# Kernel optimization log

Hardware: AMD Instinct MI355X
Metric: run time of the kernel (lower is better)

The kernel has to match this reference:

```python
import jax, jax.numpy as jnp
import numpy as np

N = 20000        # genes
E = 100000       # edges per relation
D_IN = 512
HID = 64         # hidden_dim (per-head channels in layers 0,1)
HEADS = 8
D_H = HID * HEADS   # 512 hidden width
D_OUT = 256
NEG_SLOPE = 0.2  # GATv2Conv default negative_slope


def _gatv2(x, src, dst, Wl, bl, Wr, br, att, out_bias, heads, ch):
    """PyG GATv2Conv, add_self_loops=False, concat=True, eval mode (no dropout)."""
    n = x.shape[0]
    xl = (x @ Wl + bl).reshape(n, heads, ch)   # lin_l (source transform)
    xr = (x @ Wr + br).reshape(n, heads, ch)   # lin_r (target transform)
    e = jax.nn.leaky_relu(xl[src] + xr[dst], NEG_SLOPE)   # [E,H,C]
    score = jnp.einsum('ehc,hc->eh', e, att)              # [E,H]
    # segment softmax over incoming edges of each destination node
    m = jax.ops.segment_max(score, dst, num_segments=n)   # [N,H]
    w = jnp.exp(score - m[dst])
    z = jax.ops.segment_sum(w, dst, num_segments=n)
    alpha = w / z[dst]
    out = jax.ops.segment_sum(alpha[:, :, None] * xl[src], dst, num_segments=n)
    return out.reshape(n, heads * ch) + out_bias


def _layernorm(x, g, b):
    mu = x.mean(-1, keepdims=True)
    var = x.var(-1, keepdims=True)
    return (x - mu) * jax.lax.rsqrt(var + 1e-5) * g + b


def setup_inputs() -> dict:
    key = jax.random.key(0)
    ks = jax.random.split(key, 12)
    gn = lambda k, shape, fan_in: (jax.random.normal(k, shape, dtype=jnp.float32)
                                   / np.float32(np.sqrt(fan_in)))
    inp = {}
    inp['x'] = jax.random.normal(ks[0], (N, D_IN), dtype=jnp.float32)
    inp['edge_index'] = jax.random.randint(ks[1], (3, 2, E), 0, N, dtype=jnp.int32)
    # input projection  Linear(512 -> 512)
    inp['proj_w'] = gn(ks[2], (D_IN, D_H), D_IN)
    inp['proj_b'] = jnp.zeros((D_H,), jnp.float32)
    # layers 0,1: stacked over [layer, edge_type]
    inp['l01_lin_l_w'] = gn(ks[3], (2, 3, D_H, D_H), D_H)
    inp['l01_lin_l_b'] = jnp.zeros((2, 3, D_H), jnp.float32)
    inp['l01_lin_r_w'] = gn(ks[4], (2, 3, D_H, D_H), D_H)
    inp['l01_lin_r_b'] = jnp.zeros((2, 3, D_H), jnp.float32)
    inp['l01_att'] = gn(ks[5], (2, 3, HEADS, HID), HID)
    inp['l01_bias'] = jnp.zeros((2, 3, D_H), jnp.float32)
    # layer 2: heads=1, out_channels=256, stacked over edge_type
    inp['l2_lin_l_w'] = gn(ks[6], (3, D_H, D_OUT), D_H)
    inp['l2_lin_l_b'] = jnp.zeros((3, D_OUT), jnp.float32)
    inp['l2_lin_r_w'] = gn(ks[7], (3, D_H, D_OUT), D_H)
    inp['l2_lin_r_b'] = jnp.zeros((3, D_OUT), jnp.float32)
    inp['l2_att'] = gn(ks[8], (3, 1, D_OUT), D_OUT)
    inp['l2_bias'] = jnp.zeros((3, D_OUT), jnp.float32)
    # LayerNorms
    inp['ln01_gamma'] = jnp.ones((2, D_H), jnp.float32)
    inp['ln01_beta'] = jnp.zeros((2, D_H), jnp.float32)
    inp['ln2_gamma'] = jnp.ones((D_OUT,), jnp.float32)
    inp['ln2_beta'] = jnp.zeros((D_OUT,), jnp.float32)
    return inp


def reference(x, edge_index, proj_w, proj_b,
              l01_lin_l_w, l01_lin_l_b, l01_lin_r_w, l01_lin_r_b, l01_att, l01_bias,
              l2_lin_l_w, l2_lin_l_b, l2_lin_r_w, l2_lin_r_b, l2_att, l2_bias,
              ln01_gamma, ln01_beta, ln2_gamma, ln2_beta):
    # input proj + ELU (dropout = identity in eval)
    h = jax.nn.elu(x @ proj_w + proj_b)
    # layers 0 and 1: HeteroConv(sum over 3 relations), ELU, residual, LayerNorm
    for li in range(2):
        res = h
        out = 0.0
        for et in range(3):
            src, dst = edge_index[et, 0], edge_index[et, 1]
            out = out + _gatv2(h, src, dst,
                               l01_lin_l_w[li, et], l01_lin_l_b[li, et],
                               l01_lin_r_w[li, et], l01_lin_r_b[li, et],
                               l01_att[li, et], l01_bias[li, et], HEADS, HID)
        h = jax.nn.elu(out) + res
        h = _layernorm(h, ln01_gamma[li], ln01_beta[li])
    # layer 2: heads=1, out=256; no residual (dims differ)
    out = 0.0
    for et in range(3):
        src, dst = edge_index[et, 0], edge_index[et, 1]
        out = out + _gatv2(h, src, dst,
                           l2_lin_l_w[et], l2_lin_l_b[et],
                           l2_lin_r_w[et], l2_lin_r_b[et],
                           l2_att[et], l2_bias[et], 1, D_OUT)
    h = jax.nn.elu(out)
    return _layernorm(h, ln2_gamma, ln2_beta)
```

## Files before the change

### kernel.cpp

```cpp
#include <hip/hip_runtime.h>


#define NN 20000
#define NE 100000
#define DH 512
#define DOUT 256

typedef __attribute__((ext_vector_type(8))) short short8;
typedef __attribute__((ext_vector_type(4))) short short4v;
typedef __attribute__((ext_vector_type(4))) float f32x4;

__device__ __forceinline__ float b2f(unsigned short s) {
    union { unsigned u; float f; } v; v.u = ((unsigned)s) << 16; return v.f;
}
__device__ __forceinline__ unsigned short f2b(float f) {
    unsigned u = __float_as_uint(f);
    u += 0x7FFFu + ((u >> 16) & 1u);
    return (unsigned short)(u >> 16);
}
__device__ __forceinline__ void load_lds16(const unsigned short* g, unsigned short* l) {
    __builtin_amdgcn_global_load_lds(
        (const __attribute__((address_space(1))) unsigned int*)g,
        (__attribute__((address_space(3))) unsigned int*)l, 16, 0, 0);
}

__global__ void cvt_f2b_k(const float* __restrict__ in,
                          unsigned short* __restrict__ out, int n) {
    int i0 = (blockIdx.x * blockDim.x + threadIdx.x) * 8;
    if (i0 >= n) return;
    #pragma unroll
    for (int j = 0; j < 8; j++) out[i0 + j] = f2b(in[i0 + j]);
}

__global__ void transpose_f2b_k(const float* __restrict__ in,
                                unsigned short* __restrict__ out, int R, int C,
                                long inStride, long outStride) {
    __shared__ float tile[32][33];
    in  += (size_t)blockIdx.z * inStride;
    out += (size_t)blockIdx.z * outStride;
    int c0 = blockIdx.x * 32, r0 = blockIdx.y * 32;
    int tx = threadIdx.x & 31, ty = threadIdx.x >> 5;
    #pragma unroll
    for (int i = ty; i < 32; i += 8)
        tile[i][tx] = in[(size_t)(r0 + i) * C + c0 + tx];
    __syncthreads();
    #pragma unroll
    for (int i = ty; i < 32; i += 8)
        out[(size_t)(c0 + i) * R + r0 + tx] = f2b(tile[tx][i]);
}

__global__ void count_k(const int* __restrict__ dst, int* __restrict__ counts, int E) {
    int i = blockIdx.x * blockDim.x + threadIdx.x;
    if (i < E) atomicAdd(&counts[dst[i]], 1);
}

__global__ __launch_bounds__(1024)
void scan_par_k(const int* __restrict__ counts, int* __restrict__ offs, int n) {
    __shared__ int part[1024];
    const int* c = counts + (size_t)blockIdx.x * (n + 1);
    int* o = offs + (size_t)blockIdx.x * (n + 1);
    int tid = threadIdx.x;
    int per = (n + 1023) / 1024;
    int base = tid * per;
    int lim = min(base + per, n);
    int sum = 0;
    for (int i = base; i < lim; i++) sum += c[i];
    part[tid] = sum;
    __syncthreads();
    #pragma unroll
    for (int off = 1; off < 1024; off <<= 1) {
        int v = (tid >= off) ? part[tid - off] : 0;
        __syncthreads();
        part[tid] += v;
        __syncthreads();
    }
    int run = part[tid] - sum;
    for (int i = base; i < lim; i++) { o[i] = run; run += c[i]; }
    if (tid == 1023) o[n] = part[1023];
}

__global__ void scatter_k(const int* __restrict__ src, const int* __restrict__ dst,
                          int* __restrict__ cursor, int* __restrict__ srcs_sorted, int E) {
    int i = blockIdx.x * blockDim.x + threadIdx.x;
    if (i < E) {
        int p = atomicAdd(&cursor[dst[i]], 1);
        srcs_sorted[p] = src[i];
    }
}

template<int ACT, int SEGL2>
__global__ __launch_bounds__(256)
void gemm_k(const unsigned short* __restrict__ A,
            const unsigned short* __restrict__ Bt,
            const float* __restrict__ lb,
            const float* __restrict__ rb,
            unsigned short* __restrict__ Cb,
            int M, int N, int K, int MT, int NT, int STRIPE) {
    __shared__ unsigned short As[128 * 64];
    __shared__ unsigned short Bs[128 * 64];
    int bid = blockIdx.x;
    int xcd = bid & 7, r = bid >> 3;
    int mtile = xcd * STRIPE + r / NT;
    int ntile = r % NT;
    if (mtile >= MT) return;
    int bm0 = mtile * 128, bn0 = ntile * 128;

    int tid = threadIdx.x;
    int lane = tid & 63, wave = tid >> 6;
    int quad = lane >> 4, l16 = lane & 15;
    int rw = (wave >> 1) * 64, cw = (wave & 1) * 64;
    int rxor = l16 & 7;

    f32x4 acc[4][4];
    #pragma unroll
    for (int mi = 0; mi < 4; mi++)
        #pragma unroll
        for (int ni = 0; ni < 4; ni++) acc[mi][ni] = (f32x4){0.f, 0.f, 0.f, 0.f};

    for (int k0 = 0; k0 < K; k0 += 64) {
        #pragma unroll
        for (int i = 0; i < 4; i++) {
            int f = i * 256 + tid;
            int row = f >> 3, s = f & 7;
            int cg = s ^ (row & 7);
            load_lds16(A + (size_t)(bm0 + row) * K + k0 + cg * 8, As + f * 8);
        }
        #pragma unroll
        for (int i = 0; i < 4; i++) {
            int f = i * 256 + tid;
            int col = f >> 3, s = f & 7;
            int cg = s ^ (col & 7);
            load_lds16(Bt + (size_t)(bn0 + col) * K + k0 + cg * 8, Bs + f * 8);
        }
        __syncthreads();
        #pragma unroll
        for (int ki = 0; ki < 64; ki += 32) {
            int kch = quad + (ki >> 3);
            int slot = kch ^ rxor;
            short8 af[4], bf[4];
            #pragma unroll
            for (int mi = 0; mi < 4; mi++)
                af[mi] = *(const short8*)(As + (rw + mi * 16 + l16) * 64 + slot * 8);
            #pragma unroll
            for (int ni = 0; ni < 4; ni++)
                bf[ni] = *(const short8*)(Bs + (cw + ni * 16 + l16) * 64 + slot * 8);
            #pragma unroll
            for (int mi = 0; mi < 4; mi++)
                #pragma unroll
                for (int ni = 0; ni < 4; ni++)
                    acc[mi][ni] = __builtin_amdgcn_mfma_f32_16x16x32_bf16(
                        af[mi], bf[ni], acc[mi][ni], 0, 0, 0);
        }
        __syncthreads();
    }
    #pragma unroll
    for (int mi = 0; mi < 4; mi++) {
        int orow0 = bm0 + rw + mi * 16 + quad * 4;
        #pragma unroll
        for (int ni = 0; ni < 4; ni++) {
            int col = bn0 + cw + ni * 16 + l16;
            int seg = col >> (SEGL2 + 1);
            int lr = (col >> SEGL2) & 1;
            int cc = col & ((1 << SEGL2) - 1);
            float bv = (lr ? rb : lb)[(seg << SEGL2) + cc];
            #pragma unroll
            for (int i = 0; i < 4; i++) {
                int row = orow0 + i;
                if (row >= M) continue;
                float v = acc[mi][ni][i] + bv;
                if (ACT == 1) v = v > 0.f ? v : expm1f(v);
                Cb[(size_t)row * N + col] = f2b(v);
            }
        }
    }
}

__global__ __launch_bounds__(256)
void gat_fused01_k(const unsigned short* __restrict__ C,
                   const int* __restrict__ offs3,
                   const int* __restrict__ srcs3,
                   const float* __restrict__ att,
                   const float* __restrict__ bias3,
                   unsigned short* __restrict__ hb,
                   const float* __restrict__ gamma,
                   const float* __restrict__ beta,
                   int n_nodes) {
    const unsigned LD = 3072;
    __shared__ float red[4][2];
    int tid = threadIdx.x;
    int lane = tid & 63, wave = tid >> 6;
    int half = wave & 1;
    int n = blockIdx.x * 2 + (wave >> 1);
    int c0 = half * 256 + lane * 4;
    float tot[4] = {0.f, 0.f, 0.f, 0.f};

    #pragma unroll
    for (int et = 0; et < 3; et++) {
        const int* offs = offs3 + et * (NN + 1);
        const int* srcs = srcs3 + (size_t)et * NE;
        int e0 = offs[n], e1 = offs[n + 1];
        if (e0 == e1) continue;
        const unsigned short* XL = C + et * 1024 + c0;
        float xr[4], at[4];
        {
            short4v t = *(const short4v*)(C + (size_t)n * LD + et * 1024 + 512 + c0);
            #pragma unroll
            for (int j = 0; j < 4; j++) xr[j] = b2f((unsigned short)t[j]);
            #pragma unroll
            for (int j = 0; j < 4; j++) at[j] = att[et * 512 + c0 + j];
        }
        float z = 0.f, acc[4] = {0.f, 0.f, 0.f, 0.f};
        short4v p0 = *(const short4v*)(XL + (unsigned)srcs[e0] * LD);
        short4v p1 = (e0 + 1 < e1) ? *(const short4v*)(XL + (unsigned)srcs[e0 + 1] * LD) : p0;
        for (int e = e0; e < e1; e++) {
            short4v cur = p0;
            p0 = p1;
            if (e + 2 < e1) p1 = *(const short4v*)(XL + (unsigned)srcs[e + 2] * LD);
            float xl[4];
            #pragma unroll
            for (int j = 0; j < 4; j++) xl[j] = b2f((unsigned short)cur[j]);
            float p = 0.f;
            #pragma unroll
            for (int j = 0; j < 4; j++) {
                float v = xl[j] + xr[j];
                v = v > 0.f ? v : 0.2f * v;
                p += v * at[j];
            }
            p += __shfl_xor(p, 1, 64);
            p += __shfl_xor(p, 2, 64);
            p += __shfl_xor(p, 4, 64);
            p += __shfl_xor(p, 8, 64);
            float wgt = __expf(p);
            z += wgt;
            #pragma unroll
            for (int j = 0; j < 4; j++) acc[j] += wgt * xl[j];
        }
        float inv = 1.f / z;
        #pragma unroll
        for (int j = 0; j < 4; j++) tot[j] += acc[j] * inv;
    }

    unsigned short* hrow = hb + (size_t)n * DH + c0;
    float v[4]; float s1 = 0.f;
    {
        short4v rt = *(const short4v*)hrow;
        #pragma unroll
        for (int j = 0; j < 4; j++) {
            int c = c0 + j;
            float x = tot[j] + bias3[c] + bias3[512 + c] + bias3[1024 + c];
            x = x > 0.f ? x : expm1f(x);
            x += b2f((unsigned short)rt[j]);
            v[j] = x; s1 += x;
        }
    }
    #pragma unroll
    for (int off = 1; off < 64; off <<= 1) s1 += __shfl_xor(s1, off, 64);
    if (lane == 0) red[wave][0] = s1;
    __syncthreads();
    float s1full = s1 + red[wave ^ 1][0];
    float mean = s1full * (1.f / DH);
    float s2 = 0.f;
    #pragma unroll
    for (int j = 0; j < 4; j++) { float d = v[j] - mean; s2 += d * d; }
    #pragma unroll
    for (int off = 1; off < 64; off <<= 1) s2 += __shfl_xor(s2, off, 64);
    if (lane == 0) red[wave][1] = s2;
    __syncthreads();
    float s2full = s2 + red[wave ^ 1][1];
    float rstd = rsqrtf(s2full * (1.f / DH) + 1e-5f);
    unsigned short ov[4];
    #pragma unroll
    for (int j = 0; j < 4; j++) {
        int c = c0 + j;
        ov[j] = f2b((v[j] - mean) * rstd * gamma[c] + beta[c]);
    }
    *(short4v*)hrow = (short4v){(short)ov[0], (short)ov[1], (short)ov[2], (short)ov[3]};
}

__global__ void gat_fused2_k(const unsigned short* __restrict__ C,
                             const int* __restrict__ offs3,
                             const int* __restrict__ srcs3,
                             const float* __restrict__ att,
                             const float* __restrict__ bias3,
                             const float* __restrict__ gamma,
                             const float* __restrict__ beta,
                             float* __restrict__ out, int n_nodes) {
    const unsigned LD = 1536;
    int lane = threadIdx.x & 63;
    int n = blockIdx.x * (blockDim.x >> 6) + (threadIdx.x >> 6);
    if (n >= n_nodes) return;
    int c0 = lane * 4;
    float tot[4] = {0.f, 0.f, 0.f, 0.f};

    #pragma unroll
    for (int et = 0; et < 3; et++) {
        const int* offs = offs3 + et * (NN + 1);
        const int* srcs = srcs3 + (size_t)et * NE;
        int e0 = offs[n], e1 = offs[n + 1];
        if (e0 == e1) continue;
        const unsigned short* XL = C + et * 512 + c0;
        float xr[4], at[4];
        {
            short4v t = *(const short4v*)(C + (size_t)n * LD + et * 512 + 256 + c0);
            #pragma unroll
            for (int j = 0; j < 4; j++) xr[j] = b2f((unsigned short)t[j]);
            #pragma unroll
            for (int j = 0; j < 4; j++) at[j] = att[et * 256 + c0 + j];
        }
        float z = 0.f, acc[4] = {0.f, 0.f, 0.f, 0.f};
        short4v p0 = *(const short4v*)(XL + (unsigned)srcs[e0] * LD);
        short4v p1 = (e0 + 1 < e1) ? *(const short4v*)(XL + (unsigned)srcs[e0 + 1] * LD) : p0;
        for (int e = e0; e < e1; e++) {
            short4v cur = p0;
            p0 = p1;
            if (e + 2 < e1) p1 = *(const short4v*)(XL + (unsigned)srcs[e + 2] * LD);
            float xl[4];
            #pragma unroll
            for (int j = 0; j < 4; j++) xl[j] = b2f((unsigned short)cur[j]);
            float p = 0.f;
            #pragma unroll
            for (int j = 0; j < 4; j++) {
                float v = xl[j] + xr[j];
                v = v > 0.f ? v : 0.2f * v;
                p += v * at[j];
            }
            #pragma unroll
            for (int off = 1; off < 64; off <<= 1) p += __shfl_xor(p, off, 64);
            float wgt = __expf(p);
            z += wgt;
            #pragma unroll
            for (int j = 0; j < 4; j++) acc[j] += wgt * xl[j];
        }
        float inv = 1.f / z;
        #pragma unroll
        for (int j = 0; j < 4; j++) tot[j] += acc[j] * inv;
    }

    float v[4]; float s1 = 0.f;
    #pragma unroll
    for (int j = 0; j < 4; j++) {
        int c = c0 + j;
        float x = tot[j] + bias3[c] + bias3[256 + c] + bias3[512 + c];
        x = x > 0.f ? x : expm1f(x);
        v[j] = x; s1 += x;
    }
    #pragma unroll
    for (int off = 1; off < 64; off <<= 1) s1 += __shfl_xor(s1, off, 64);
    float mean = s1 * (1.f / DOUT);
    float s2 = 0.f;
    #pragma unroll
    for (int j = 0; j < 4; j++) { float d = v[j] - mean; s2 += d * d; }
    #pragma unroll
    for (int off = 1; off < 64; off <<= 1) s2 += __shfl_xor(s2, off, 64);
    float rstd = rsqrtf(s2 * (1.f / DOUT) + 1e-5f);
    #pragma unroll
    for (int j = 0; j < 4; j++) {
        int c = c0 + j;
        out[(size_t)n * DOUT + c] = (v[j] - mean) * rstd * gamma[c] + beta[c];
    }
}

extern "C" void kernel_launch(void* const* d_in, const int* in_sizes, int n_in,
                              void* d_out, int out_size, void* d_ws, size_t ws_size,
                              hipStream_t stream) {
    const float* x       = (const float*)d_in[0];
    const int*   ei      = (const int*)d_in[1];
    const float* proj_w  = (const float*)d_in[2];
    const float* proj_b  = (const float*)d_in[3];
    const float* l01lw   = (const float*)d_in[4];
    const float* l01lb   = (const float*)d_in[5];
    const float* l01rw   = (const float*)d_in[6];
    const float* l01rb   = (const float*)d_in[7];
    const float* l01att  = (const float*)d_in[8];
    const float* l01bias = (const float*)d_in[9];
    const float* l2lw    = (const float*)d_in[10];
    const float* l2lb    = (const float*)d_in[11];
    const float* l2rw    = (const float*)d_in[12];
    const float* l2rb    = (const float*)d_in[13];
    const float* l2att   = (const float*)d_in[14];
    const float* l2bias  = (const float*)d_in[15];
    const float* g01     = (const float*)d_in[16];
    const float* b01     = (const float*)d_in[17];
    const float* g2      = (const float*)d_in[18];
    const float* b2      = (const float*)d_in[19];
    (void)in_sizes; (void)n_in; (void)out_size; (void)ws_size;

    char* w = (char*)d_ws;
    size_t off = 0;
    auto carve = [&](size_t bytes) { void* p = w + off; off = (off + bytes + 255) & ~(size_t)255; return p; };
    unsigned short* h_b     = (unsigned short*)carve((size_t)NN * DH * 2);
    unsigned short* xb      = (unsigned short*)carve((size_t)NN * DH * 2);
    unsigned short* Cbuf    = (unsigned short*)carve((size_t)NN * 3072 * 2);
    unsigned short* Wt      = (unsigned short*)carve((size_t)4194304 * 2);
    int*            counts3 = (int*)           carve((size_t)3 * (NN + 1) * 4);
    int*            offs3   = (int*)           carve((size_t)3 * (NN + 1) * 4);
    int*            srcs3   = (int*)           carve((size_t)3 * NE * 4);
    carve(65536);

    unsigned short* Wt_proj = Wt;
    unsigned short* Wt_L0   = Wt_proj + 262144;
    unsigned short* Wt_L1   = Wt_L0 + 3072 * 512;
    unsigned short* Wt_L2   = Wt_L1 + 3072 * 512;

    dim3 tb(256);
    const int MT = (NN + 127) / 128;
    const int STRIPE = (MT + 7) / 8;

    cvt_f2b_k<<<dim3(5000), tb, 0, stream>>>(x, xb, NN * DH);
    transpose_f2b_k<<<dim3(16, 16, 1), tb, 0, stream>>>(proj_w, Wt_proj, 512, 512, 0, 0);
    for (int li = 0; li < 2; li++) {
        unsigned short* base = li ? Wt_L1 : Wt_L0;
        transpose_f2b_k<<<dim3(16, 16, 3), tb, 0, stream>>>(
            l01lw + (size_t)li * 3 * 262144, base, 512, 512, 262144, 2 * 262144);
        transpose_f2b_k<<<dim3(16, 16, 3), tb, 0, stream>>>(
            l01rw + (size_t)li * 3 * 262144, base + 262144, 512, 512, 262144, 2 * 262144);
    }
    transpose_f2b_k<<<dim3(8, 16, 3), tb, 0, stream>>>(
        l2lw, Wt_L2, 512, 256, 131072, 2 * 131072);
    transpose_f2b_k<<<dim3(8, 16, 3), tb, 0, stream>>>(
        l2rw, Wt_L2 + 131072, 512, 256, 131072, 2 * 131072);

    hipMemsetAsync(counts3, 0, (size_t)3 * (NN + 1) * 4, stream);
    for (int et = 0; et < 3; et++) {
        const int* dst = ei + (size_t)et * 2 * NE + NE;
        count_k<<<dim3((NE + 255) / 256), tb, 0, stream>>>(dst, counts3 + et * (NN + 1), NE);
    }
    scan_par_k<<<dim3(3), dim3(1024), 0, stream>>>(counts3, offs3, NN);
    hipMemcpyAsync(counts3, offs3, (size_t)3 * (NN + 1) * 4,
                   hipMemcpyDeviceToDevice, stream);
    for (int et = 0; et < 3; et++) {
        const int* src = ei + (size_t)et * 2 * NE;
        const int* dst = src + NE;
        scatter_k<<<dim3((NE + 255) / 256), tb, 0, stream>>>(
            src, dst, counts3 + et * (NN + 1), srcs3 + (size_t)et * NE, NE);
    }

    gemm_k<1, 9><<<dim3(8 * STRIPE * 4), tb, 0, stream>>>(
        xb, Wt_proj, proj_b, proj_b, h_b, NN, 512, 512, MT, 4, STRIPE);

    for (int li = 0; li < 2; li++) {
        gemm_k<0, 9><<<dim3(8 * STRIPE * 24), tb, 0, stream>>>(
            h_b, li ? Wt_L1 : Wt_L0,
            l01lb + (size_t)li * 3 * 512, l01rb + (size_t)li * 3 * 512,
            Cbuf, NN, 3072, 512, MT, 24, STRIPE);
        gat_fused01_k<<<dim3(NN / 2), tb, 0, stream>>>(
            Cbuf, offs3, srcs3,
            l01att + (size_t)li * 3 * 512, l01bias + (size_t)li * 3 * 512,
            h_b, g01 + (size_t)li * DH, b01 + (size_t)li * DH, NN);
    }

    gemm_k<0, 8><<<dim3(8 * STRIPE * 12), tb, 0, stream>>>(
        h_b, Wt_L2, l2lb, l2rb, Cbuf, NN, 1536, 512, MT, 12, STRIPE);
    gat_fused2_k<<<dim3(NN / 4), tb, 0, stream>>>(
        Cbuf, offs3, srcs3, l2att, l2bias, g2, b2, (float*)d_out, NN);
}
```

Before: 766.5 us.

## Batch weight transposes and CSR builds into single launches; stage GEMM stores via LDS

Merges the many per-weight transpose launches into one table-driven kernel, and folds the per-relation count and scatter launches into single kernels covering all three relations. This is meant to cut kernel launch overhead in the preprocessing phase. The GEMM epilogue now writes bf16 results into a padded LDS tile and stores rows back with 16-byte vector writes instead of scattered 2-byte stores. That should improve write coalescing, at the cost of a larger shared buffer (about 34 KB) and an extra barrier.

```diff
diff --git a/kernel.cpp b/kernel.cpp
--- a/kernel.cpp
+++ b/kernel.cpp
@@ -32,26 +32,33 @@
     for (int j = 0; j < 8; j++) out[i0 + j] = f2b(in[i0 + j]);
 }
 
-__global__ void transpose_f2b_k(const float* __restrict__ in,
-                                unsigned short* __restrict__ out, int R, int C,
-                                long inStride, long outStride) {
+struct TSeg { const float* in; unsigned short* out; int C; };
+struct TTable { TSeg s[19]; };
+
+__global__ void transpose_all_k(TTable t) {
     __shared__ float tile[32][33];
-    in  += (size_t)blockIdx.z * inStride;
-    out += (size_t)blockIdx.z * outStride;
-    int c0 = blockIdx.x * 32, r0 = blockIdx.y * 32;
+    TSeg d = t.s[blockIdx.y];
+    int tiles_x = d.C >> 5;
+    int nt = tiles_x << 4;
+    if ((int)blockIdx.x >= nt) return;
+    int bx = blockIdx.x % tiles_x, by = blockIdx.x / tiles_x;
+    int c0 = bx * 32, r0 = by * 32;
     int tx = threadIdx.x & 31, ty = threadIdx.x >> 5;
     #pragma unroll
     for (int i = ty; i < 32; i += 8)
-        tile[i][tx] = in[(size_t)(r0 + i) * C + c0 + tx];
+        tile[i][tx] = d.in[(size_t)(r0 + i) * d.C + c0 + tx];
     __syncthreads();
     #pragma unroll
     for (int i = ty; i < 32; i += 8)
-        out[(size_t)(c0 + i) * R + r0 + tx] = f2b(tile[tx][i]);
-}
-
-__global__ void count_k(const int* __restrict__ dst, int* __restrict__ counts, int E) {
+        d.out[(size_t)(c0 + i) * 512 + r0 + tx] = f2b(tile[tx][i]);
+}
+
+__global__ void count_all_k(const int* __restrict__ ei, int* __restrict__ counts) {
     int i = blockIdx.x * blockDim.x + threadIdx.x;
-    if (i < E) atomicAdd(&counts[dst[i]], 1);
+    if (i >= 3 * NE) return;
+    int et = i / NE, idx = i - et * NE;
+    int d = ei[(size_t)et * 2 * NE + NE + idx];
+    atomicAdd(&counts[et * (NN + 1) + d], 1);
 }
 
 __global__ __launch_bounds__(1024)
@@ -79,13 +86,15 @@
     if (tid == 1023) o[n] = part[1023];
 }
 
-__global__ void scatter_k(const int* __restrict__ src, const int* __restrict__ dst,
-                          int* __restrict__ cursor, int* __restrict__ srcs_sorted, int E) {
+__global__ void scatter_all_k(const int* __restrict__ ei, int* __restrict__ cursor,
+                              int* __restrict__ srcs_sorted) {
     int i = blockIdx.x * blockDim.x + threadIdx.x;
-    if (i < E) {
-        int p = atomicAdd(&cursor[dst[i]], 1);
-        srcs_sorted[p] = src[i];
-    }
+    if (i >= 3 * NE) return;
+    int et = i / NE, idx = i - et * NE;
+    int s = ei[(size_t)et * 2 * NE + idx];
+    int d = ei[(size_t)et * 2 * NE + NE + idx];
+    int p = atomicAdd(&cursor[et * (NN + 1) + d], 1);
+    srcs_sorted[(size_t)et * NE + p] = s;
 }
 
 template<int ACT, int SEGL2>
@@ -96,8 +105,9 @@
             const float* __restrict__ rb,
             unsigned short* __restrict__ Cb,
             int M, int N, int K, int MT, int NT, int STRIPE) {
-    __shared__ unsigned short As[128 * 64];
-    __shared__ unsigned short Bs[128 * 64];
+    __shared__ __align__(16) unsigned short smem[17408];
+    unsigned short* As = smem;
+    unsigned short* Bs = smem + 8192;
     int bid = blockIdx.x;
     int xcd = bid & 7, r = bid >> 3;
     int mtile = xcd * STRIPE + r / NT;
@@ -153,24 +163,34 @@
         }
         __syncthreads();
     }
-    #pragma unroll
-    for (int mi = 0; mi < 4; mi++) {
-        int orow0 = bm0 + rw + mi * 16 + quad * 4;
-        #pragma unroll
-        for (int ni = 0; ni < 4; ni++) {
-            int col = bn0 + cw + ni * 16 + l16;
-            int seg = col >> (SEGL2 + 1);
-            int lr = (col >> SEGL2) & 1;
-            int cc = col & ((1 << SEGL2) - 1);
-            float bv = (lr ? rb : lb)[(seg << SEGL2) + cc];
+
+    #pragma unroll
+    for (int ni = 0; ni < 4; ni++) {
+        int col = cw + ni * 16 + l16;
+        int seg = col >> (SEGL2 + 1);
+        int lr = (col >> SEGL2) & 1;
+        int cc2 = col & ((1 << SEGL2) - 1);
+        float bv = (lr ? rb : lb)[(seg << SEGL2) + cc2];
+        #pragma unroll
+        for (int mi = 0; mi < 4; mi++) {
+            int row = rw + mi * 16 + quad * 4;
             #pragma unroll
             for (int i = 0; i < 4; i++) {
-                int row = orow0 + i;
-                if (row >= M) continue;
                 float v = acc[mi][ni][i] + bv;
                 if (ACT == 1) v = v > 0.f ? v : expm1f(v);
-                Cb[(size_t)row * N + col] = f2b(v);
+                smem[(row + i) * 136 + col] = f2b(v);
             }
+        }
+    }
+    __syncthreads();
+    #pragma unroll
+    for (int it = 0; it < 8; it++) {
+        int chunk = it * 256 + tid;
+        int row = chunk >> 4, cc = chunk & 15;
+        int grow = bm0 + row;
+        if (grow < M) {
+            uint4 d = *(const uint4*)(smem + row * 136 + cc * 8);
+            *(uint4*)(Cb + (size_t)grow * N + bn0 + cc * 8) = d;
         }
     }
 }
@@ -407,33 +427,34 @@
     const int STRIPE = (MT + 7) / 8;
 
     cvt_f2b_k<<<dim3(5000), tb, 0, stream>>>(x, xb, NN * DH);
-    transpose_f2b_k<<<dim3(16, 16, 1), tb, 0, stream>>>(proj_w, Wt_proj, 512, 512, 0, 0);
-    for (int li = 0; li < 2; li++) {
-        unsigned short* base = li ? Wt_L1 : Wt_L0;
-        transpose_f2b_k<<<dim3(16, 16, 3), tb, 0, stream>>>(
-            l01lw + (size_t)li * 3 * 262144, base, 512, 512, 262144, 2 * 262144);
-        transpose_f2b_k<<<dim3(16, 16, 3), tb, 0, stream>>>(
-            l01rw + (size_t)li * 3 * 262144, base + 262144, 512, 512, 262144, 2 * 262144);
-    }
-    transpose_f2b_k<<<dim3(8, 16, 3), tb, 0, stream>>>(
-        l2lw, Wt_L2, 512, 256, 131072, 2 * 131072);
-    transpose_f2b_k<<<dim3(8, 16, 3), tb, 0, stream>>>(
-        l2rw, Wt_L2 + 131072, 512, 256, 131072, 2 * 131072);
+    TTable tt;
+    {
+        int s = 0;
+        tt.s[s++] = {proj_w, Wt_proj, 512};
+        for (int li = 0; li < 2; li++) {
+            unsigned short* base = li ? Wt_L1 : Wt_L0;
+            for (int et = 0; et < 3; et++)
+                tt.s[s++] = {l01lw + (size_t)(li * 3 + et) * 262144,
+                             base + (size_t)et * 2 * 262144, 512};
+            for (int et = 0; et < 3; et++)
+                tt.s[s++] = {l01rw + (size_t)(li * 3 + et) * 262144,
+                             base + 262144 + (size_t)et * 2 * 262144, 512};
+        }
+        for (int et = 0; et < 3; et++)
+            tt.s[s++] = {l2lw + (size_t)et * 131072,
+                         Wt_L2 + (size_t)et * 2 * 131072, 256};
+        for (int et = 0; et < 3; et++)
+            tt.s[s++] = {l2rw + (size_t)et * 131072,
+                         Wt_L2 + 131072 + (size_t)et * 2 * 131072, 256};
+    }
+    transpose_all_k<<<dim3(256, 19), tb, 0, stream>>>(tt);
 
     hipMemsetAsync(counts3, 0, (size_t)3 * (NN + 1) * 4, stream);
-    for (int et = 0; et < 3; et++) {
-        const int* dst = ei + (size_t)et * 2 * NE + NE;
-        count_k<<<dim3((NE + 255) / 256), tb, 0, stream>>>(dst, counts3 + et * (NN + 1), NE);
-    }
+    count_all_k<<<dim3((3 * NE + 255) / 256), tb, 0, stream>>>(ei, counts3);
     scan_par_k<<<dim3(3), dim3(1024), 0, stream>>>(counts3, offs3, NN);
     hipMemcpyAsync(counts3, offs3, (size_t)3 * (NN + 1) * 4,
                    hipMemcpyDeviceToDevice, stream);
-    for (int et = 0; et < 3; et++) {
-        const int* src = ei + (size_t)et * 2 * NE;
-        const int* dst = src + NE;
-        scatter_k<<<dim3((NE + 255) / 256), tb, 0, stream>>>(
-            src, dst, counts3 + et * (NN + 1), srcs3 + (size_t)et * NE, NE);
-    }
+    scatter_all_k<<<dim3((3 * NE + 255) / 256), tb, 0, stream>>>(ei, counts3, srcs3);
 
     gemm_k<1, 9><<<dim3(8 * STRIPE * 4), tb, 0, stream>>>(
         xb, Wt_proj, proj_b, proj_b, h_b, NN, 512, 512, MT, 4, STRIPE);
```

Result: faster. 666.6 us (-13.0%).
